# Performance work log

Measured on AMD Instinct MI355X. Metric: run time of the kernel, lower is better.

## Reference

```python
import jax, jax.numpy as jnp
import numpy as np

B, T, Q, H = 128, 50, 1024, 256
MAX_STEP = 50
TEMP = 0.5
SUP_W, DIST_W, EMBED_W, LOSS_WEIGHT = 1.0, 0.01, 1.0, 1.0
BLUR, DIAMETER, REACH, SCALING, P = 0.005, 1.0, 500.0, 0.5, 2
NEG = -1e9


def _softmin(eps, C, h):
    # h: log-weights + potential/eps over the second axis of C
    return -eps * jax.nn.logsumexp(h[None, :] - C / eps, axis=1)


def _sqcost(u, v):
    sq = jnp.sum(u * u, -1)[:, None] + jnp.sum(v * v, -1)[None, :] - 2.0 * (u @ v.T)
    return 0.5 * jnp.maximum(sq, 0.0)  # geomloss p=2 cost: |x-y|^2 / 2


def sinkhorn_divergence(x, y):
    # geomloss SamplesLoss('sinkhorn', p=2, blur=0.005, diameter=1, reach=500),
    # tensorized, debiased, unbalanced, eps-scaling schedule.
    N, M = x.shape[0], y.shape[0]
    a_log = jnp.full((N,), -np.log(float(N)), dtype=x.dtype)
    b_log = jnp.full((M,), -np.log(float(M)), dtype=x.dtype)
    Cxy, Cyx = _sqcost(x, y), _sqcost(y, x)
    Cxx, Cyy = _sqcost(x, x), _sqcost(y, y)
    rho = REACH ** P
    eps_final = BLUR ** P
    eps_list = []
    e = DIAMETER ** P
    while e > eps_final:
        eps_list.append(e)
        e = e * (SCALING ** P)
    eps_list.append(eps_final)
    f_ab = jnp.zeros((N,), x.dtype)
    g_ab = jnp.zeros((M,), x.dtype)
    f_aa = jnp.zeros((N,), x.dtype)
    g_bb = jnp.zeros((M,), x.dtype)
    for eps in eps_list:  # static schedule (~9 steps)
        damp = 1.0 / (1.0 + eps / rho)
        ft = damp * _softmin(eps, Cxy, b_log + g_ab / eps)
        gt = damp * _softmin(eps, Cyx, a_log + f_ab / eps)
        faa = 0.5 * (f_aa + damp * _softmin(eps, Cxx, a_log + f_aa / eps))
        gbb = 0.5 * (g_bb + damp * _softmin(eps, Cyy, b_log + g_bb / eps))
        f_ab, g_ab, f_aa, g_bb = ft, gt, faa, gbb
    w = rho + eps_final / 2.0  # UnbalancedWeight
    a_w, b_w = jnp.exp(a_log), jnp.exp(b_log)
    return (jnp.sum(a_w * w * (jnp.exp(-f_aa / rho) - jnp.exp(-f_ab / rho)))
            + jnp.sum(b_w * w * (jnp.exp(-g_bb / rho) - jnp.exp(-g_ab / rho))))


def _forward(lc, lt, le, ltc, ltt, lte, ohs, oht, ods, odt, batch):
    p_c, p_t, p_e = lc / TEMP, lt / TEMP, le / TEMP
    q_c, q_t, q_e = ltc / TEMP, ltt / TEMP, lte / TEMP
    flat = lambda z: z.reshape(z.shape[0], -1)
    loss_kd = (sinkhorn_divergence(flat(p_c), flat(q_c))
               + sinkhorn_divergence(flat(p_t), flat(q_t))
               + sinkhorn_divergence(flat(p_e), flat(q_e)))
    S = MAX_STEP - 1
    delta = batch[:, :, :Q] + batch[:, :, Q:]  # [B,T,Q] question one-hots
    a = jnp.floor(((batch[:, :, :Q] - batch[:, :, Q:]).sum(-1) + 1.0) / 2.0)[:, 1:1 + S]  # [B,S] correctness
    dsh = delta[:, 1:1 + S]  # [B,S,Q]
    # diagonal of p[:S] @ delta[1:].T == per-step gather of next question's logit
    pc = jnp.einsum('bsq,bsq->bs', p_c[:, :S], dsh)
    pt = jnp.einsum('bsq,bsq->bs', p_t[:, :S], dsh)
    pe = jnp.einsum('bsq,bsq->bs', p_e[:, :S], dsh)
    idx = jnp.arange(S)
    last = jnp.max(jnp.where(pc > 0, idx[None, :], -1), axis=1)  # last i with pc[i] > 0
    L = jnp.where(last >= 0, last + 1, S)  # no break => keep full length
    mask = idx[None, :] < L[:, None]
    def ce(logits):
        m = jnp.where(mask, logits, NEG)
        lsm = m - jax.nn.logsumexp(m, axis=1, keepdims=True)
        return -jnp.sum(jnp.where(mask, a * lsm, 0.0))  # soft-target CE, summed over students
    loss_sup = ce(pt) + ce(pc) + ce(pe)
    embed = 0.5 * (jnp.sum((ohs - oht) ** 2) + jnp.sum((ods - odt) ** 2))
    total = LOSS_WEIGHT * (SUP_W * loss_sup + DIST_W * loss_kd + EMBED_W * embed)
    return total.reshape(1)


def setup_inputs():
    key = jax.random.key(0)
    ks = jax.random.split(key, 12)
    rn = lambda k, s: jax.random.normal(k, s, dtype=jnp.float32)
    qid = jax.random.randint(ks[10], (B, T), 0, Q)
    correct = jax.random.randint(ks[11], (B, T), 0, 2).astype(jnp.float32)
    oh = jax.nn.one_hot(qid, Q, dtype=jnp.float32)
    batch = jnp.concatenate([oh * correct[..., None], oh * (1.0 - correct)[..., None]], axis=-1)
    return {
        'logit_c': rn(ks[0], (B, T, Q)),
        'logit_t': rn(ks[1], (B, T, Q)),
        'logit_ensemble': rn(ks[2], (B, T, Q)),
        'logit_teacher_c': rn(ks[3], (B, T, Q)),
        'logit_teacher_t': rn(ks[4], (B, T, Q)),
        'logit_teacher_ensemble': rn(ks[5], (B, T, Q)),
        'out_h_student': rn(ks[6], (B, T, H)),
        'out_h_teacher': rn(ks[7], (B, T, H)),
        'out_d_student': rn(ks[8], (B, T, H)),
        'out_d_teacher': rn(ks[9], (B, T, H)),
        'batch': batch,
    }


def reference(logit_c, logit_t, logit_ensemble, logit_teacher_c, logit_teacher_t, logit_teacher_ensemble, out_h_student, out_h_teacher, out_d_student, out_d_teacher, batch):
    return _forward(logit_c, logit_t, logit_ensemble, logit_teacher_c, logit_teacher_t, logit_teacher_ensemble, out_h_student, out_h_teacher, out_d_student, out_d_teacher, batch)
```

## Files before the change

### kernel.cpp

```cpp
#include <hip/hip_runtime.h>

#define NB 128
#define T_DIM 50
#define Q_DIM 1024
#define H_DIM 256
#define S_DIM 49
#define K_DIM 51200
#define KCHUNKS 80
#define KC 640
#define BK 64
#define NSTAGE 10
#define GRAM_N (NB * NB)
#define LROWU 36

typedef __attribute__((ext_vector_type(4))) float f32x4;
typedef __attribute__((ext_vector_type(8))) _Float16 half8v;
typedef __attribute__((ext_vector_type(4))) unsigned int uint4v;
typedef __attribute__((ext_vector_type(2))) unsigned int uint2v;
using pk2_t = decltype(__builtin_amdgcn_cvt_pkrtz(0.0f, 0.0f));

union PKU { pk2_t p; unsigned int u; };
union U4H8 { uint4v u; half8v h; };

__device__ inline unsigned short f2bf_rn(float x) {
  union { float f; unsigned int u; } v; v.f = x;
  unsigned int r = v.u + 0x7FFFu + ((v.u >> 16) & 1u);
  return (unsigned short)(r >> 16);
}
__device__ inline float bf2f(unsigned short b) {
  union { float f; unsigned int u; } v; v.u = ((unsigned int)b) << 16;
  return v.f;
}

__global__ __launch_bounds__(1024) void gram_fused_kernel(
    const float* __restrict__ s0, const float* __restrict__ s1, const float* __restrict__ s2,
    const float* __restrict__ t0, const float* __restrict__ t1, const float* __restrict__ t2,
    unsigned short* __restrict__ part) {
  __shared__ unsigned int panA[NB * LROWU];
  __shared__ unsigned int panB[NB * LROWU];

  const int chunk = blockIdx.x;
  const int pair = blockIdx.y;
  const float* S  = (pair == 0) ? s0 : ((pair == 1) ? s1 : s2);
  const float* Tm = (pair == 0) ? t0 : ((pair == 1) ? t1 : t2);

  const int tid = threadIdx.x;
  const int wave = tid >> 6, lane = tid & 63;
  const int wrow = wave >> 2, wcol = wave & 3;
  const int l15 = lane & 15, quad = lane >> 4;

  f32x4 aXY[2][2], aXX[2][2], aYY[2][2];
#pragma unroll
  for (int i = 0; i < 2; i++)
#pragma unroll
    for (int j = 0; j < 2; j++) {
      aXY[i][j] = (f32x4){0.f, 0.f, 0.f, 0.f};
      aXX[i][j] = (f32x4){0.f, 0.f, 0.f, 0.f};
      aYY[i][j] = (f32x4){0.f, 0.f, 0.f, 0.f};
    }

  const int r0 = tid >> 4;
  const int kq = tid & 15;
  const size_t ro0 = (size_t)r0 * K_DIM;
  const size_t ro1 = (size_t)(r0 + 64) * K_DIM;

  const int kbase = chunk * KC;
  f32x4 pre0, pre1, pre2, pre3;

#define ISSUE_LOADS(KPOS)                                    \
  {                                                          \
    const float* pS = S + (KPOS) + kq * 4;                   \
    const float* pT = Tm + (KPOS) + kq * 4;                  \
    pre0 = *(const f32x4*)(pS + ro0);                        \
    pre1 = *(const f32x4*)(pS + ro1);                        \
    pre2 = *(const f32x4*)(pT + ro0);                        \
    pre3 = *(const f32x4*)(pT + ro1);                        \
  }

  ISSUE_LOADS(kbase)

  for (int st = 0; st < NSTAGE; st++) {
    if (st) __syncthreads();
    {
      PKU a, b; uint2v w;
      a.p = __builtin_amdgcn_cvt_pkrtz(pre0[0], pre0[1]);
      b.p = __builtin_amdgcn_cvt_pkrtz(pre0[2], pre0[3]);
      w.x = a.u; w.y = b.u;
      *(uint2v*)&panA[r0 * LROWU + kq * 2] = w;
      a.p = __builtin_amdgcn_cvt_pkrtz(pre1[0], pre1[1]);
      b.p = __builtin_amdgcn_cvt_pkrtz(pre1[2], pre1[3]);
      w.x = a.u; w.y = b.u;
      *(uint2v*)&panA[(r0 + 64) * LROWU + kq * 2] = w;
      a.p = __builtin_amdgcn_cvt_pkrtz(pre2[0], pre2[1]);
      b.p = __builtin_amdgcn_cvt_pkrtz(pre2[2], pre2[3]);
      w.x = a.u; w.y = b.u;
      *(uint2v*)&panB[r0 * LROWU + kq * 2] = w;
      a.p = __builtin_amdgcn_cvt_pkrtz(pre3[0], pre3[1]);
      b.p = __builtin_amdgcn_cvt_pkrtz(pre3[2], pre3[3]);
      w.x = a.u; w.y = b.u;
      *(uint2v*)&panB[(r0 + 64) * LROWU + kq * 2] = w;
    }
    __syncthreads();
    if (st + 1 < NSTAGE) ISSUE_LOADS(kbase + (st + 1) * BK)

#pragma unroll
    for (int ks = 0; ks < 2; ks++) {
      const int kc = ks * 16 + quad * 4;
      half8v as_[2], bs_[2], at_[2], bt_[2];
#pragma unroll
      for (int t = 0; t < 2; t++) {
        U4H8 u;
        u.u = *(const uint4v*)&panA[(wrow * 32 + t * 16 + l15) * LROWU + kc]; as_[t] = u.h;
        u.u = *(const uint4v*)&panA[(wcol * 32 + t * 16 + l15) * LROWU + kc]; bs_[t] = u.h;
        u.u = *(const uint4v*)&panB[(wrow * 32 + t * 16 + l15) * LROWU + kc]; at_[t] = u.h;
        u.u = *(const uint4v*)&panB[(wcol * 32 + t * 16 + l15) * LROWU + kc]; bt_[t] = u.h;
      }
#pragma unroll
      for (int ti = 0; ti < 2; ti++)
#pragma unroll
        for (int tj = 0; tj < 2; tj++) {
          aXY[ti][tj] = __builtin_amdgcn_mfma_f32_16x16x32_f16(as_[ti], bt_[tj], aXY[ti][tj], 0, 0, 0);
          aXX[ti][tj] = __builtin_amdgcn_mfma_f32_16x16x32_f16(as_[ti], bs_[tj], aXX[ti][tj], 0, 0, 0);
          aYY[ti][tj] = __builtin_amdgcn_mfma_f32_16x16x32_f16(at_[ti], bt_[tj], aYY[ti][tj], 0, 0, 0);
        }
    }
  }
#undef ISSUE_LOADS

#pragma unroll
  for (int kind = 0; kind < 3; kind++) {
    unsigned short* out = part + ((size_t)(pair * 3 + kind) * KCHUNKS + chunk) * GRAM_N;
#pragma unroll
    for (int ti = 0; ti < 2; ti++)
#pragma unroll
      for (int tj = 0; tj < 2; tj++) {
        const f32x4 v = (kind == 0) ? aXY[ti][tj] : ((kind == 1) ? aXX[ti][tj] : aYY[ti][tj]);
        const int col = wcol * 32 + tj * 16 + l15;
#pragma unroll
        for (int r = 0; r < 4; r++) {
          const int row = wrow * 32 + ti * 16 + quad * 4 + r;
          out[(size_t)row * NB + col] = f2bf_rn(v[r]);
        }
      }
  }
}

__global__ __launch_bounds__(256) void gram_reduce_kernel(
    const unsigned short* __restrict__ part, float* __restrict__ gram) {
  const int idx = blockIdx.x * 256 + threadIdx.x;
  const int g = idx >> 14;
  const int cell = idx & (GRAM_N - 1);
  const unsigned short* p = part + (size_t)g * KCHUNKS * GRAM_N + cell;
  float s = 0.f;
#pragma unroll
  for (int c = 0; c < KCHUNKS; c++) s += bf2f(p[(size_t)c * GRAM_N]);
  gram[idx] = s;
}

__global__ __launch_bounds__(256) void sinkhorn_part_kernel(
    const float* __restrict__ gram, float* __restrict__ kdpart) {
  const int pair = blockIdx.x, kind = blockIdx.y;
  const float* Gxy = gram + (size_t)(3 * pair + 0) * GRAM_N;
  const float* Gxx = gram + (size_t)(3 * pair + 1) * GRAM_N;
  const float* Gyy = gram + (size_t)(3 * pair + 2) * GRAM_N;

  __shared__ unsigned short C[NB][132];
  __shared__ float nx[NB], ny[NB];
  __shared__ float pot0[NB], pot1[NB];
  __shared__ float np0[NB], np1[NB];
  __shared__ float red[256];

  const int tid = threadIdx.x;
  if (tid < NB) {
    nx[tid] = Gxx[tid * (NB + 1)];
    ny[tid] = Gyy[tid * (NB + 1)];
    pot0[tid] = 0.f; pot1[tid] = 0.f;
  }
  __syncthreads();

  const float* G  = (kind == 0) ? Gxy : ((kind == 1) ? Gxx : Gyy);
  const float* rn = (kind == 2) ? ny : nx;
  const float* cn = (kind == 1) ? nx : ny;
  for (int idx = tid; idx < GRAM_N; idx += 256) {
    const int i = idx >> 7, j = idx & 127;
    const float c = 2.0f * fmaxf(rn[i] + cn[j] - 2.0f * G[idx], 0.0f);
    C[i][j] = f2bf_rn(c);
  }
  __syncthreads();

  const float rho = 250000.0f;
  const float AL = -4.852030263919617f;
  const int grp = tid >> 7;
  const int i = tid & 127;
  const bool active = (kind == 0) ? true : (grp == 0);
  const bool colread = (kind == 0) && (grp == 1);

  float eps = 1.0f;
  for (int it = 0; it < 9; it++) {
    if (it == 8) eps = 2.5e-5f;
    const float inv_eps = 1.0f / eps;
    const float damp = 1.0f / (1.0f + eps / rho);
    const float ebl = eps * AL;

    if (active) {
      const float* h = (kind == 0 && grp == 0) ? pot1 : pot0;
      float m0 = -3.0e38f, m1 = -3.0e38f, m2 = -3.0e38f, m3 = -3.0e38f;
      float s0 = 0.f, s1 = 0.f, s2 = 0.f, s3 = 0.f;
      for (int j = 0; j < NB; j += 4) {
        float c0, c1, c2, c3;
        if (colread) {
          c0 = bf2f(C[j + 0][i]); c1 = bf2f(C[j + 1][i]);
          c2 = bf2f(C[j + 2][i]); c3 = bf2f(C[j + 3][i]);
        } else {
          c0 = bf2f(C[i][j + 0]); c1 = bf2f(C[i][j + 1]);
          c2 = bf2f(C[i][j + 2]); c3 = bf2f(C[i][j + 3]);
        }
        const float u0 = ebl + h[j + 0] - c0;
        const float u1 = ebl + h[j + 1] - c1;
        const float u2 = ebl + h[j + 2] - c2;
        const float u3 = ebl + h[j + 3] - c3;
        float nm;
        nm = fmaxf(m0, u0); s0 = s0 * __expf((m0 - nm) * inv_eps) + __expf((u0 - nm) * inv_eps); m0 = nm;
        nm = fmaxf(m1, u1); s1 = s1 * __expf((m1 - nm) * inv_eps) + __expf((u1 - nm) * inv_eps); m1 = nm;
        nm = fmaxf(m2, u2); s2 = s2 * __expf((m2 - nm) * inv_eps) + __expf((u2 - nm) * inv_eps); m2 = nm;
        nm = fmaxf(m3, u3); s3 = s3 * __expf((m3 - nm) * inv_eps) + __expf((u3 - nm) * inv_eps); m3 = nm;
      }
      const float M = fmaxf(fmaxf(m0, m1), fmaxf(m2, m3));
      const float Ssum = s0 * __expf((m0 - M) * inv_eps) + s1 * __expf((m1 - M) * inv_eps)
                       + s2 * __expf((m2 - M) * inv_eps) + s3 * __expf((m3 - M) * inv_eps);
      const float sm = -(M + eps * __logf(Ssum));
      float newp;
      if (kind == 0) newp = damp * sm;
      else           newp = 0.5f * (pot0[i] + damp * sm);
      if (grp == 0) np0[i] = newp; else np1[i] = newp;
    }
    __syncthreads();
    if (tid < NB) {
      pot0[tid] = np0[tid];
      if (kind == 0) pot1[tid] = np1[tid];
    }
    __syncthreads();
    eps *= 0.25f;
  }

  float v = 0.f;
  if (kind == 0) {
    v = (grp == 0) ? -__expf(-pot0[i] / rho)
                   : -__expf(-pot1[i] / rho);
  } else if (grp == 0) {
    v = __expf(-pot0[i] / rho);
  }
  red[tid] = v;
  __syncthreads();
  for (int st = 128; st > 0; st >>= 1) {
    if (tid < st) red[tid] += red[tid + st];
    __syncthreads();
  }
  if (tid == 0) kdpart[pair * 3 + kind] = red[0];
}

__global__ __launch_bounds__(256) void ps_kernel(
    const float* __restrict__ lc, const float* __restrict__ lt, const float* __restrict__ le,
    const float* __restrict__ batch,
    float* __restrict__ pc, float* __restrict__ pt, float* __restrict__ pe,
    float* __restrict__ aarr) {
  const int bs = blockIdx.x;
  const int b = bs / S_DIM, s = bs % S_DIM;
  const float* brow = batch + ((size_t)b * T_DIM + (s + 1)) * (2 * Q_DIM);
  __shared__ int sq;
  __shared__ float sds;
  if (threadIdx.x == 0) sq = 0;
  __syncthreads();
  for (int q = threadIdx.x; q < Q_DIM; q += 256) {
    float d0 = brow[q], d1 = brow[Q_DIM + q];
    if (d0 + d1 > 0.5f) { sq = q; sds = d0 - d1; }
  }
  __syncthreads();
  if (threadIdx.x == 0) {
    const size_t off = ((size_t)b * T_DIM + s) * Q_DIM + sq;
    pc[bs] = 2.0f * lc[off];
    pt[bs] = 2.0f * lt[off];
    pe[bs] = 2.0f * le[off];
    aarr[bs] = (sds > 0.0f) ? 1.0f : 0.0f;
  }
}

__global__ __launch_bounds__(256) void embed_kernel(
    const f32x4* __restrict__ hs, const f32x4* __restrict__ ht,
    const f32x4* __restrict__ ds, const f32x4* __restrict__ dt,
    float* __restrict__ acc) {
  const int N4 = NB * T_DIM * H_DIM / 4;
  float sum = 0.f;
  for (int idx = blockIdx.x * 256 + threadIdx.x; idx < N4; idx += gridDim.x * 256) {
    f32x4 a = hs[idx] - ht[idx];
    f32x4 b = ds[idx] - dt[idx];
    sum += a[0]*a[0] + a[1]*a[1] + a[2]*a[2] + a[3]*a[3]
         + b[0]*b[0] + b[1]*b[1] + b[2]*b[2] + b[3]*b[3];
  }
  for (int off = 32; off > 0; off >>= 1) sum += __shfl_down(sum, off, 64);
  __shared__ float wsum[4];
  const int lane = threadIdx.x & 63, wv = threadIdx.x >> 6;
  if (lane == 0) wsum[wv] = sum;
  __syncthreads();
  if (threadIdx.x == 0) atomicAdd(acc, wsum[0] + wsum[1] + wsum[2] + wsum[3]);
}

__device__ inline float ce_row(const float* __restrict__ x, const float* __restrict__ a, int L) {
  float m = -3.0e38f;
  for (int s = 0; s < L; s++) m = fmaxf(m, x[s]);
  float sum = 0.f;
  for (int s = 0; s < L; s++) sum += __expf(x[s] - m);
  const float lse = m + __logf(sum);
  float loss = 0.f;
  for (int s = 0; s < L; s++) loss += a[s] * (x[s] - lse);
  return -loss;
}

__global__ __launch_bounds__(128) void ce_final_kernel(
    const float* __restrict__ pc, const float* __restrict__ pt, const float* __restrict__ pe,
    const float* __restrict__ aarr, const float* __restrict__ kdpart,
    const float* __restrict__ emb, float* __restrict__ out) {
  const int b = threadIdx.x;
  const float* xc = pc + b * S_DIM;
  const float* xt = pt + b * S_DIM;
  const float* xe = pe + b * S_DIM;
  const float* av = aarr + b * S_DIM;
  int last = -1;
  for (int s = 0; s < S_DIM; s++)
    if (xc[s] > 0.0f) last = s;
  const int L = (last >= 0) ? (last + 1) : S_DIM;
  float loss = ce_row(xt, av, L) + ce_row(xc, av, L) + ce_row(xe, av, L);
  __shared__ float red[128];
  red[b] = loss;
  __syncthreads();
  for (int st = 64; st > 0; st >>= 1) {
    if (b < st) red[b] += red[b + st];
    __syncthreads();
  }
  if (b == 0) {
    float kd = 0.f;
    for (int k = 0; k < 9; k++) kd += kdpart[k];
    out[0] = red[0] + 0.01f * (250000.0000125f / 128.0f) * kd + 0.5f * emb[0];
  }
}

extern "C" void kernel_launch(void* const* d_in, const int* in_sizes, int n_in,
                              void* d_out, int out_size, void* d_ws, size_t ws_size,
                              hipStream_t stream) {
  const float* lc    = (const float*)d_in[0];
  const float* lt    = (const float*)d_in[1];
  const float* le    = (const float*)d_in[2];
  const float* ltc   = (const float*)d_in[3];
  const float* ltt   = (const float*)d_in[4];
  const float* lte   = (const float*)d_in[5];
  const float* ohs   = (const float*)d_in[6];
  const float* oht   = (const float*)d_in[7];
  const float* ods   = (const float*)d_in[8];
  const float* odt   = (const float*)d_in[9];
  const float* batch = (const float*)d_in[10];

  unsigned short* part = (unsigned short*)d_ws;
  float* gram = (float*)(part + (size_t)9 * KCHUNKS * GRAM_N);
  float* pcb  = gram + 9 * GRAM_N;
  float* ptb  = pcb + NB * S_DIM;
  float* peb  = ptb + NB * S_DIM;
  float* ab   = peb + NB * S_DIM;
  float* kdp  = ab + NB * S_DIM;
  float* emb  = kdp + 9;

  hipMemsetAsync(emb, 0, sizeof(float), stream);

  embed_kernel<<<512, 256, 0, stream>>>(
      (const f32x4*)ohs, (const f32x4*)oht, (const f32x4*)ods, (const f32x4*)odt, emb);

  ps_kernel<<<NB * S_DIM, 256, 0, stream>>>(lc, lt, le, batch, pcb, ptb, peb, ab);

  gram_fused_kernel<<<dim3(KCHUNKS, 3), 1024, 0, stream>>>(lc, lt, le, ltc, ltt, lte, part);

  gram_reduce_kernel<<<(9 * GRAM_N) / 256, 256, 0, stream>>>(part, gram);

  sinkhorn_part_kernel<<<dim3(3, 3), 256, 0, stream>>>(gram, kdp);

  ce_final_kernel<<<1, 128, 0, stream>>>(pcb, ptb, peb, ab, kdp, emb, (float*)d_out);
}
```

Before: 377.0 us.

## Cache Sinkhorn cost rows in registers and use two-pass logsumexp

```diff
diff --git a/kernel.cpp b/kernel.cpp
--- a/kernel.cpp
+++ b/kernel.cpp
@@ -12,6 +12,7 @@
 #define NSTAGE 10
 #define GRAM_N (NB * NB)
 #define LROWU 36
+#define CPAD 132
 
 typedef __attribute__((ext_vector_type(4))) float f32x4;
 typedef __attribute__((ext_vector_type(8))) _Float16 half8v;
@@ -157,24 +158,25 @@
   gram[idx] = s;
 }
 
-__global__ __launch_bounds__(256) void sinkhorn_part_kernel(
+__global__ __launch_bounds__(256, 1) void sinkhorn_part_kernel(
     const float* __restrict__ gram, float* __restrict__ kdpart) {
   const int pair = blockIdx.x, kind = blockIdx.y;
   const float* Gxy = gram + (size_t)(3 * pair + 0) * GRAM_N;
   const float* Gxx = gram + (size_t)(3 * pair + 1) * GRAM_N;
   const float* Gyy = gram + (size_t)(3 * pair + 2) * GRAM_N;
 
-  __shared__ unsigned short C[NB][132];
+  __shared__ float CL[NB * CPAD];
+  __shared__ f32x4 h4a[NB / 4];
+  __shared__ f32x4 h4b[NB / 4];
   __shared__ float nx[NB], ny[NB];
-  __shared__ float pot0[NB], pot1[NB];
-  __shared__ float np0[NB], np1[NB];
   __shared__ float red[256];
 
   const int tid = threadIdx.x;
   if (tid < NB) {
     nx[tid] = Gxx[tid * (NB + 1)];
     ny[tid] = Gyy[tid * (NB + 1)];
-    pot0[tid] = 0.f; pot1[tid] = 0.f;
+    ((float*)h4a)[tid] = 0.f;
+    ((float*)h4b)[tid] = 0.f;
   }
   __syncthreads();
 
@@ -183,17 +185,37 @@
   const float* cn = (kind == 1) ? nx : ny;
   for (int idx = tid; idx < GRAM_N; idx += 256) {
     const int i = idx >> 7, j = idx & 127;
-    const float c = 2.0f * fmaxf(rn[i] + cn[j] - 2.0f * G[idx], 0.0f);
-    C[i][j] = f2bf_rn(c);
+    CL[i * CPAD + j] = 2.0f * fmaxf(rn[i] + cn[j] - 2.0f * G[idx], 0.0f);
   }
   __syncthreads();
 
   const float rho = 250000.0f;
   const float AL = -4.852030263919617f;
+  const float LOG2E = 1.4426950408889634f;
+  const float LN2 = 0.6931471805599453f;
   const int grp = tid >> 7;
   const int i = tid & 127;
-  const bool active = (kind == 0) ? true : (grp == 0);
+  const bool active = (kind == 0) || (grp == 0);
   const bool colread = (kind == 0) && (grp == 1);
+
+  f32x4 crow[32];
+  if (active) {
+    if (colread) {
+#pragma unroll
+      for (int jj = 0; jj < 32; jj++) {
+        f32x4 v;
+        v[0] = CL[(4 * jj + 0) * CPAD + i];
+        v[1] = CL[(4 * jj + 1) * CPAD + i];
+        v[2] = CL[(4 * jj + 2) * CPAD + i];
+        v[3] = CL[(4 * jj + 3) * CPAD + i];
+        crow[jj] = v;
+      }
+    } else {
+#pragma unroll
+      for (int jj = 0; jj < 32; jj++)
+        crow[jj] = *(const f32x4*)&CL[i * CPAD + 4 * jj];
+    }
+  }
 
   float eps = 1.0f;
   for (int it = 0; it < 9; it++) {
@@ -202,42 +224,36 @@
     const float damp = 1.0f / (1.0f + eps / rho);
     const float ebl = eps * AL;
 
+    float newp = 0.f;
     if (active) {
-      const float* h = (kind == 0 && grp == 0) ? pot1 : pot0;
-      float m0 = -3.0e38f, m1 = -3.0e38f, m2 = -3.0e38f, m3 = -3.0e38f;
-      float s0 = 0.f, s1 = 0.f, s2 = 0.f, s3 = 0.f;
-      for (int j = 0; j < NB; j += 4) {
-        float c0, c1, c2, c3;
-        if (colread) {
-          c0 = bf2f(C[j + 0][i]); c1 = bf2f(C[j + 1][i]);
-          c2 = bf2f(C[j + 2][i]); c3 = bf2f(C[j + 3][i]);
-        } else {
-          c0 = bf2f(C[i][j + 0]); c1 = bf2f(C[i][j + 1]);
-          c2 = bf2f(C[i][j + 2]); c3 = bf2f(C[i][j + 3]);
-        }
-        const float u0 = ebl + h[j + 0] - c0;
-        const float u1 = ebl + h[j + 1] - c1;
-        const float u2 = ebl + h[j + 2] - c2;
-        const float u3 = ebl + h[j + 3] - c3;
-        float nm;
-        nm = fmaxf(m0, u0); s0 = s0 * __expf((m0 - nm) * inv_eps) + __expf((u0 - nm) * inv_eps); m0 = nm;
-        nm = fmaxf(m1, u1); s1 = s1 * __expf((m1 - nm) * inv_eps) + __expf((u1 - nm) * inv_eps); m1 = nm;
-        nm = fmaxf(m2, u2); s2 = s2 * __expf((m2 - nm) * inv_eps) + __expf((u2 - nm) * inv_eps); m2 = nm;
-        nm = fmaxf(m3, u3); s3 = s3 * __expf((m3 - nm) * inv_eps) + __expf((u3 - nm) * inv_eps); m3 = nm;
+      const f32x4* h = (kind == 0 && grp == 0) ? h4b : h4a;
+      f32x4 m4 = (f32x4){-3.0e38f, -3.0e38f, -3.0e38f, -3.0e38f};
+#pragma unroll
+      for (int jj = 0; jj < 32; jj++) {
+        const f32x4 u = h[jj] - crow[jj];
+        m4[0] = fmaxf(m4[0], u[0]); m4[1] = fmaxf(m4[1], u[1]);
+        m4[2] = fmaxf(m4[2], u[2]); m4[3] = fmaxf(m4[3], u[3]);
       }
-      const float M = fmaxf(fmaxf(m0, m1), fmaxf(m2, m3));
-      const float Ssum = s0 * __expf((m0 - M) * inv_eps) + s1 * __expf((m1 - M) * inv_eps)
-                       + s2 * __expf((m2 - M) * inv_eps) + s3 * __expf((m3 - M) * inv_eps);
-      const float sm = -(M + eps * __logf(Ssum));
-      float newp;
+      const float m = fmaxf(fmaxf(m4[0], m4[1]), fmaxf(m4[2], m4[3]));
+      const float k = inv_eps * LOG2E;
+      f32x4 s4 = (f32x4){0.f, 0.f, 0.f, 0.f};
+#pragma unroll
+      for (int jj = 0; jj < 32; jj++) {
+        const f32x4 u = h[jj] - crow[jj];
+        s4[0] += __builtin_exp2f((u[0] - m) * k);
+        s4[1] += __builtin_exp2f((u[1] - m) * k);
+        s4[2] += __builtin_exp2f((u[2] - m) * k);
+        s4[3] += __builtin_exp2f((u[3] - m) * k);
+      }
+      const float Ssum = (s4[0] + s4[1]) + (s4[2] + s4[3]);
+      const float sm = -(m + ebl + eps * (LN2 * __log2f(Ssum)));
       if (kind == 0) newp = damp * sm;
-      else           newp = 0.5f * (pot0[i] + damp * sm);
-      if (grp == 0) np0[i] = newp; else np1[i] = newp;
+      else           newp = 0.5f * (((const float*)h4a)[i] + damp * sm);
     }
     __syncthreads();
-    if (tid < NB) {
-      pot0[tid] = np0[tid];
-      if (kind == 0) pot1[tid] = np1[tid];
+    if (active) {
+      if (grp == 0) ((float*)h4a)[i] = newp;
+      else          ((float*)h4b)[i] = newp;
     }
     __syncthreads();
     eps *= 0.25f;
@@ -245,10 +261,10 @@
 
   float v = 0.f;
   if (kind == 0) {
-    v = (grp == 0) ? -__expf(-pot0[i] / rho)
-                   : -__expf(-pot1[i] / rho);
+    v = (grp == 0) ? -__expf(-((const float*)h4a)[i] / rho)
+                   : -__expf(-((const float*)h4b)[i] / rho);
   } else if (grp == 0) {
-    v = __expf(-pot0[i] / rho);
+    v = __expf(-((const float*)h4a)[i] / rho);
   }
   red[tid] = v;
   __syncthreads();
```

After: 362.4 us. -3.9%, faster.
